# Kernel optimization log

Measured on AMD Instinct MI355X. Metric: run time of the kernel, lower is better.

## Reference

```python
import jax, jax.numpy as jnp
import numpy as np

N_NODES = 40000
N_EDGES = 640000
IN_DIM, H_DIM, OUT_DIM = 128, 128, 64


def setup_inputs() -> dict:
    key = jax.random.key(0)
    ks = jax.random.split(key, 16)
    x = jax.random.normal(ks[0], (N_NODES, IN_DIM), dtype=jnp.float32)
    edge_index = jax.random.randint(ks[1], (2, N_EDGES), 0, N_NODES, dtype=jnp.int64)
    dims = [(IN_DIM, H_DIM), (H_DIM, H_DIM), (H_DIM, OUT_DIM)]
    inp = {"x": x, "edge_index": edge_index}
    for l, (di, do) in enumerate(dims):
        s = 1.0 / np.sqrt(di)
        inp[f"Wr{l}"] = jax.random.uniform(ks[2 + 3 * l], (di, do), jnp.float32, -s, s)  # lin_rel weight
        inp[f"br{l}"] = jax.random.uniform(ks[3 + 3 * l], (do,), jnp.float32, -s, s)     # lin_rel bias
        inp[f"Ws{l}"] = jax.random.uniform(ks[4 + 3 * l], (di, do), jnp.float32, -s, s)  # lin_root weight (no bias)
    return inp


def _graph_conv(x, src, dst, Wr, br, Ws):
    # PyG GraphConv (aggr='add'): out = lin_rel(sum_{j in N(i)} x_j) + lin_root(x_i)
    agg = jax.ops.segment_sum(x[src], dst, num_segments=N_NODES)  # [N, d_in]
    return agg @ Wr + br + x @ Ws


def reference(x, edge_index, Wr0, br0, Ws0, Wr1, br1, Ws1, Wr2, br2, Ws2):
    src, dst = edge_index[0], edge_index[1]
    h = x
    for Wr, br, Ws in ((Wr0, br0, Ws0), (Wr1, br1, Ws1), (Wr2, br2, Ws2)):
        h = _graph_conv(h, src, dst, Wr, br, Ws)
        h = jax.nn.relu(h)
        # dropout p=0 / eval mode -> identity
    return jax.nn.log_softmax(h, axis=1)
```

## Files before the change

### kernel.cpp

```cpp
#include <hip/hip_runtime.h>
#include <hip/hip_bf16.h>


#define N_NODES 40000
#define N_EDGES 640000
#define PAD_NODES 40064
#define DEG_CAP   40960
#define ROW_CAP   64

typedef float v4f __attribute__((ext_vector_type(4)));
typedef float v2f __attribute__((ext_vector_type(2)));
typedef short short8 __attribute__((ext_vector_type(8)));

__device__ inline unsigned short f2b(float f) {
    unsigned u = __float_as_uint(f);
    return (unsigned short)((u + 0x7fffu + ((u >> 16) & 1u)) >> 16);
}

__device__ inline unsigned b2f8(unsigned short us) {
    unsigned s  = ((unsigned)us >> 8) & 0x80u;
    unsigned mag = us & 0x7fffu;
    unsigned e8 = mag >> 7, m7 = mag & 0x7fu;
    unsigned out;
    if (e8 < 121u) out = 0u;
    else if (e8 > 135u) out = 0x7eu;
    else {
        unsigned e4 = e8 - 120u;
        unsigned r  = (m7 + 7u + ((m7 >> 4) & 1u)) >> 4;
        if (r == 8u) { r = 0u; e4++; }
        out = (e4 > 15u || (e4 == 15u && r > 6u)) ? 0x7eu : ((e4 << 3) | r);
    }
    return s | out;
}

#if __has_builtin(__builtin_amdgcn_cvt_f32_fp8)
#define F8TOF(w, sel) __builtin_amdgcn_cvt_f32_fp8((int)(w), (sel))
#else
__device__ inline float f8tof_(unsigned b) {
    unsigned e = (b >> 3) & 15u;
    unsigned bits = ((b & 0x80u) << 24) |
                    (e ? (((e + 120u) << 23) | ((b & 7u) << 20)) : 0u);
    return __uint_as_float(bits);
}
#define F8TOF(w, sel) f8tof_(((unsigned)(w) >> ((sel) * 8)) & 0xffu)
#endif

__global__ __launch_bounds__(256) void prep_kernel(const float* __restrict__ Wr0, const float* __restrict__ Ws0,
                                                   const float* __restrict__ Wr1, const float* __restrict__ Ws1,
                                                   const float* __restrict__ Wr2, const float* __restrict__ Ws2,
                                                   unsigned short* __restrict__ Wt0,
                                                   unsigned short* __restrict__ Wt1,
                                                   unsigned short* __restrict__ Wt2,
                                                   int* __restrict__ deg) {
    int tid = blockIdx.x * 256 + threadIdx.x;
    if (tid < DEG_CAP / 4) {
        ((int4*)deg)[tid] = make_int4(0, 0, 0, 0);
    } else {
        int t = tid - DEG_CAP / 4;
        if (t < 32768) {
            int n = t >> 7, k = t & 127;
            const float* W = (n < 128) ? Wr0 : Ws0;
            Wt0[t] = f2b(W[k * 128 + (n & 127)]);
        } else if (t < 65536) {
            int u = t - 32768;
            int n = u >> 7, k = u & 127;
            const float* W = (n < 128) ? Wr1 : Ws1;
            Wt1[u] = f2b(W[k * 128 + (n & 127)]);
        } else if (t < 81920) {
            int u = t - 65536;
            int n = u >> 7, k = u & 127;
            const float* W = (n < 64) ? Wr2 : Ws2;
            Wt2[u] = f2b(W[k * 64 + (n & 63)]);
        }
    }
}

__global__ __launch_bounds__(256) void place_kernel(const int* __restrict__ src,
                                                    const int* __restrict__ dst,
                                                    int* __restrict__ deg,
                                                    int* __restrict__ esrc) {
    int e = blockIdx.x * 256 + threadIdx.x;
    if (e < N_EDGES) {
        int d = dst[e];
        int r = atomicAdd(&deg[d], 1);
        if (r < ROW_CAP) esrc[(size_t)d * ROW_CAP + r] = src[e];
    }
}

template <int DO, bool F32>
__global__ __launch_bounds__(256, 3) void mm_kernel(const void* __restrict__ Ain,
                                                    const unsigned short* __restrict__ Wt,
                                                    void* __restrict__ Tout,
                                                    unsigned short* __restrict__ S) {
    __shared__ unsigned short Smem[128 * 128];
    unsigned short* As = Smem;
    unsigned short* Bs = Smem + 128 * 64;

    const int tid = threadIdx.x;
    const int m0  = blockIdx.x * 128;
    const int n0  = blockIdx.y * 128;

    const int wave = tid >> 6;
    const int lane = tid & 63;
    const int wr   = (wave >> 1) * 64;
    const int wc   = (wave & 1) * 64;
    const int qm   = lane & 15;
    const int k8   = (lane >> 4) * 8;

    v4f acc[4][4];
#pragma unroll
    for (int i = 0; i < 4; i++)
#pragma unroll
        for (int j = 0; j < 4; j++) acc[i][j] = (v4f)(0.0f);

#pragma unroll
    for (int half = 0; half < 2; half++) {
        if (F32) {
            const float4* Xg = (const float4*)Ain;
#pragma unroll
            for (int i = 0; i < 8; i++) {
                int idx = i * 256 + tid;
                int row = idx >> 4, c4 = idx & 15;
                int gr = m0 + row;
                if (gr > N_NODES - 1) gr = N_NODES - 1;
                float4 v = Xg[(size_t)gr * 32 + half * 16 + c4];
                uint2 p;
                p.x = (unsigned)f2b(v.x) | ((unsigned)f2b(v.y) << 16);
                p.y = (unsigned)f2b(v.z) | ((unsigned)f2b(v.w) << 16);
                ((uint2*)As)[idx] = p;
            }
        } else {
            const unsigned short* Ab = (const unsigned short*)Ain;
#pragma unroll
            for (int i = 0; i < 4; i++) {
                int idx = i * 256 + tid;
                int row = idx >> 3, c8 = idx & 7;
                ((uint4*)As)[idx] =
                    *(const uint4*)(Ab + (size_t)(m0 + row) * 128 + half * 64 + c8 * 8);
            }
        }
        {
#pragma unroll
            for (int i = 0; i < 4; i++) {
                int idx = i * 256 + tid;
                int row = idx >> 3, c8 = idx & 7;
                ((uint4*)Bs)[idx] =
                    *(const uint4*)(Wt + (size_t)(n0 + row) * 128 + half * 64 + c8 * 8);
            }
        }
        __syncthreads();

#pragma unroll
        for (int ks = 0; ks < 2; ks++) {
            short8 af[4], bf[4];
#pragma unroll
            for (int i = 0; i < 4; i++) {
                af[i] = *(const short8*)(const void*)(As + (wr + i * 16 + qm) * 64 + ks * 32 + k8);
                bf[i] = *(const short8*)(const void*)(Bs + (wc + i * 16 + qm) * 64 + ks * 32 + k8);
            }
#pragma unroll
            for (int mi = 0; mi < 4; mi++)
#pragma unroll
                for (int ni = 0; ni < 4; ni++)
                    acc[mi][ni] = __builtin_amdgcn_mfma_f32_16x16x32_bf16(af[mi], bf[ni], acc[mi][ni], 0, 0, 0);
        }
        __syncthreads();
    }

#pragma unroll
    for (int mi = 0; mi < 4; mi++) {
        const int rowBase = wr + mi * 16 + ((lane >> 4) << 2);
#pragma unroll
        for (int r = 0; r < 4; r++) {
            const int row = rowBase + r;
            const int sw  = ((row >> 2) & 3) << 4;
#pragma unroll
            for (int ni = 0; ni < 4; ni++) {
                const int c = wc + ni * 16 + qm;
                Smem[row * 128 + (c ^ sw)] = f2b(acc[mi][ni][r]);
            }
        }
    }
    __syncthreads();

    if (DO == 128 && n0 == 0) {
        unsigned char* T8 = (unsigned char*)Tout;
#pragma unroll
        for (int i = 0; i < 4; i++) {
            const int chunk = i * 256 + tid;
            const int row   = chunk >> 3;
            const int c0    = (chunk & 7) * 16;
            const int sw    = ((row >> 2) & 3) << 4;
            const int node  = m0 + row;
            if (node <= N_NODES) {
                uint4 v = make_uint4(0, 0, 0, 0);
                if (node < N_NODES) {
                    const unsigned short* p = Smem + row * 128 + (c0 ^ sw);
                    unsigned wds[4];
#pragma unroll
                    for (int w4 = 0; w4 < 4; w4++) {
                        wds[w4] =  b2f8(p[w4 * 4 + 0])
                                | (b2f8(p[w4 * 4 + 1]) << 8)
                                | (b2f8(p[w4 * 4 + 2]) << 16)
                                | (b2f8(p[w4 * 4 + 3]) << 24);
                    }
                    v = make_uint4(wds[0], wds[1], wds[2], wds[3]);
                }
                *(uint4*)(T8 + (size_t)node * 128 + c0) = v;
            }
        }
    } else {
        unsigned short* T = (unsigned short*)Tout;
#pragma unroll
        for (int i = 0; i < 8; i++) {
            const int chunk = i * 256 + tid;
            const int row   = chunk >> 4;
            const int c0    = (chunk & 15) * 8;
            const int sw    = ((row >> 2) & 3) << 4;
            const int node  = m0 + row;
            if (node <= N_NODES) {
                uint4 v = make_uint4(0, 0, 0, 0);
                if (node < N_NODES)
                    v = *(const uint4*)(Smem + row * 128 + (c0 ^ sw));
                if (DO == 128) {
                    *(uint4*)(S + (size_t)node * 128 + c0) = v;
                } else {
                    if (c0 < 64) *(uint4*)(T + (size_t)node * 64 + c0) = v;
                    else         *(uint4*)(S + (size_t)node * 64 + (c0 - 64)) = v;
                }
            }
        }
    }
}

__device__ inline void addp(v2f* a, uint4 q) {
    v2f t0 = { __uint_as_float(q.x << 16), __uint_as_float(q.x & 0xffff0000u) };
    v2f t1 = { __uint_as_float(q.y << 16), __uint_as_float(q.y & 0xffff0000u) };
    v2f t2 = { __uint_as_float(q.z << 16), __uint_as_float(q.z & 0xffff0000u) };
    v2f t3 = { __uint_as_float(q.w << 16), __uint_as_float(q.w & 0xffff0000u) };
    a[0] += t0; a[1] += t1; a[2] += t2; a[3] += t3;
}
__device__ inline void addp8(v2f* a, uint2 q) {
    v2f t0 = { F8TOF(q.x, 0), F8TOF(q.x, 1) };
    v2f t1 = { F8TOF(q.x, 2), F8TOF(q.x, 3) };
    v2f t2 = { F8TOF(q.y, 0), F8TOF(q.y, 1) };
    v2f t3 = { F8TOF(q.y, 2), F8TOF(q.y, 3) };
    a[0] += t0; a[1] += t1; a[2] += t2; a[3] += t3;
}

template <int DO, bool LAST, bool FP8T>
__global__ __launch_bounds__(256) void aggregate_kernel(const void* __restrict__ Tin,
                                                        const unsigned short* __restrict__ S,
                                                        const float* __restrict__ br,
                                                        const int* __restrict__ deg,
                                                        const int* __restrict__ esrc,
                                                        unsigned short* __restrict__ Hout,
                                                        float* __restrict__ Fout) {
    constexpr int TPN = DO / 8;
    constexpr int G   = 256 / TPN;
    const int lane = threadIdx.x % TPN;
    const int n    = blockIdx.x * G + threadIdx.x / TPN;

    int cnt = deg[n];
    if (cnt > ROW_CAP) cnt = ROW_CAP;
    const int* erow = esrc + (size_t)n * ROW_CAP;
    const uint4* T4 = (const uint4*)Tin;
    const uint2* T2 = (const uint2*)Tin;

    const uint4  sv = ((const uint4*)S)[(size_t)n * TPN + lane];
    const float4 b0 = ((const float4*)br)[lane * 2];
    const float4 b1 = ((const float4*)br)[lane * 2 + 1];

    v2f acc[4];
    acc[0] = (v2f)(0.0f); acc[1] = (v2f)(0.0f);
    acc[2] = (v2f)(0.0f); acc[3] = (v2f)(0.0f);

    for (int o = 0; o < cnt; o += 8) {
        int4 i0 = *(const int4*)(erow + o);
        int4 i1 = *(const int4*)(erow + o + 4);
        i0.x = (o + 0 < cnt) ? i0.x : N_NODES;
        i0.y = (o + 1 < cnt) ? i0.y : N_NODES;
        i0.z = (o + 2 < cnt) ? i0.z : N_NODES;
        i0.w = (o + 3 < cnt) ? i0.w : N_NODES;
        i1.x = (o + 4 < cnt) ? i1.x : N_NODES;
        i1.y = (o + 5 < cnt) ? i1.y : N_NODES;
        i1.z = (o + 6 < cnt) ? i1.z : N_NODES;
        i1.w = (o + 7 < cnt) ? i1.w : N_NODES;
        if (FP8T) {
            uint2 q0 = T2[(size_t)i0.x * TPN + lane];
            uint2 q1 = T2[(size_t)i0.y * TPN + lane];
            uint2 q2 = T2[(size_t)i0.z * TPN + lane];
            uint2 q3 = T2[(size_t)i0.w * TPN + lane];
            uint2 q4 = T2[(size_t)i1.x * TPN + lane];
            uint2 q5 = T2[(size_t)i1.y * TPN + lane];
            uint2 q6 = T2[(size_t)i1.z * TPN + lane];
            uint2 q7 = T2[(size_t)i1.w * TPN + lane];
            addp8(acc, q0); addp8(acc, q1); addp8(acc, q2); addp8(acc, q3);
            addp8(acc, q4); addp8(acc, q5); addp8(acc, q6); addp8(acc, q7);
        } else {
            uint4 q0 = T4[(size_t)i0.x * TPN + lane];
            uint4 q1 = T4[(size_t)i0.y * TPN + lane];
            uint4 q2 = T4[(size_t)i0.z * TPN + lane];
            uint4 q3 = T4[(size_t)i0.w * TPN + lane];
            uint4 q4 = T4[(size_t)i1.x * TPN + lane];
            uint4 q5 = T4[(size_t)i1.y * TPN + lane];
            uint4 q6 = T4[(size_t)i1.z * TPN + lane];
            uint4 q7 = T4[(size_t)i1.w * TPN + lane];
            addp(acc, q0); addp(acc, q1); addp(acc, q2); addp(acc, q3);
            addp(acc, q4); addp(acc, q5); addp(acc, q6); addp(acc, q7);
        }
    }
    addp(acc, sv);

    float v[8];
    v[0] = fmaxf(acc[0].x + b0.x, 0.f); v[1] = fmaxf(acc[0].y + b0.y, 0.f);
    v[2] = fmaxf(acc[1].x + b0.z, 0.f); v[3] = fmaxf(acc[1].y + b0.w, 0.f);
    v[4] = fmaxf(acc[2].x + b1.x, 0.f); v[5] = fmaxf(acc[2].y + b1.y, 0.f);
    v[6] = fmaxf(acc[3].x + b1.z, 0.f); v[7] = fmaxf(acc[3].y + b1.w, 0.f);

    if (LAST) {
        float m = v[0];
#pragma unroll
        for (int i = 1; i < 8; i++) m = fmaxf(m, v[i]);
#pragma unroll
        for (int off = 4; off; off >>= 1) m = fmaxf(m, __shfl_xor(m, off, 64));
        float es = 0.f;
#pragma unroll
        for (int i = 0; i < 8; i++) es += expf(v[i] - m);
#pragma unroll
        for (int off = 4; off; off >>= 1) es += __shfl_xor(es, off, 64);
        float lse = m + logf(es);
        float4 o0 = make_float4(v[0] - lse, v[1] - lse, v[2] - lse, v[3] - lse);
        float4 o1 = make_float4(v[4] - lse, v[5] - lse, v[6] - lse, v[7] - lse);
        ((float4*)Fout)[(size_t)n * 16 + lane * 2]     = o0;
        ((float4*)Fout)[(size_t)n * 16 + lane * 2 + 1] = o1;
    } else {
        uint4 o;
        o.x = (unsigned)f2b(v[0]) | ((unsigned)f2b(v[1]) << 16);
        o.y = (unsigned)f2b(v[2]) | ((unsigned)f2b(v[3]) << 16);
        o.z = (unsigned)f2b(v[4]) | ((unsigned)f2b(v[5]) << 16);
        o.w = (unsigned)f2b(v[6]) | ((unsigned)f2b(v[7]) << 16);
        ((uint4*)Hout)[(size_t)n * TPN + lane] = o;
    }
}


extern "C" void kernel_launch(void* const* d_in, const int* in_sizes, int n_in,
                              void* d_out, int out_size, void* d_ws, size_t ws_size,
                              hipStream_t stream) {
    const float* x    = (const float*)d_in[0];
    const int*   eidx = (const int*)d_in[1];
    const float* Wr0  = (const float*)d_in[2];
    const float* br0  = (const float*)d_in[3];
    const float* Ws0  = (const float*)d_in[4];
    const float* Wr1  = (const float*)d_in[5];
    const float* br1  = (const float*)d_in[6];
    const float* Ws1  = (const float*)d_in[7];
    const float* Wr2  = (const float*)d_in[8];
    const float* br2  = (const float*)d_in[9];
    const float* Ws2  = (const float*)d_in[10];
    float* out = (float*)d_out;

    const int* src = eidx;
    const int* dst = eidx + N_EDGES;

    auto align = [](size_t v) { return (v + 255) & ~(size_t)255; };
    char* w = (char*)d_ws;
    int* deg  = (int*)w;  w += align(sizeof(int) * DEG_CAP);
    int* esrc = (int*)w;  w += align(sizeof(int) * (size_t)N_NODES * ROW_CAP);
    unsigned short* H1b = (unsigned short*)w;  w += align(2ull * PAD_NODES * 128);
    unsigned short* H2b = (unsigned short*)w;  w += align(2ull * PAD_NODES * 128);
    unsigned short* Wt0 = (unsigned short*)w;  w += align(2ull * 256 * 128);
    unsigned short* Wt1 = (unsigned short*)w;  w += align(2ull * 256 * 128);
    unsigned short* Wt2 = (unsigned short*)w;  w += align(2ull * 128 * 128);
    void*           T   = (void*)w;            w += align(2ull * PAD_NODES * 128);
    unsigned short* Sb  = (unsigned short*)w;  w += align(2ull * PAD_NODES * 128);
    (void)ws_size; (void)n_in; (void)in_sizes; (void)out_size;

    prep_kernel<<<(DEG_CAP / 4 + 81920 + 255) / 256, 256, 0, stream>>>(
        Wr0, Ws0, Wr1, Ws1, Wr2, Ws2, Wt0, Wt1, Wt2, deg);

    place_kernel<<<(N_EDGES + 255) / 256, 256, 0, stream>>>(src, dst, deg, esrc);

    mm_kernel<128, true><<<dim3(PAD_NODES / 128, 2), 256, 0, stream>>>(x, Wt0, T, Sb);
    aggregate_kernel<128, false, true><<<N_NODES / 16, 256, 0, stream>>>(T, Sb, br0, deg, esrc, H1b, nullptr);

    mm_kernel<128, false><<<dim3(PAD_NODES / 128, 2), 256, 0, stream>>>(H1b, Wt1, T, Sb);
    aggregate_kernel<128, false, true><<<N_NODES / 16, 256, 0, stream>>>(T, Sb, br1, deg, esrc, H2b, nullptr);

    mm_kernel<64, false><<<dim3(PAD_NODES / 128, 1), 256, 0, stream>>>(H2b, Wt2, T, Sb);
    aggregate_kernel<64, true, false><<<N_NODES / 32, 256, 0, stream>>>(T, Sb, br2, deg, esrc, nullptr, out);
}
```

Baseline: 212.5 us.

## Pre-convert x to bf16, use hardware fp8 packing, widen aggregate gathers

```diff
diff --git a/kernel.cpp b/kernel.cpp
--- a/kernel.cpp
+++ b/kernel.cpp
@@ -33,6 +33,17 @@
     return s | out;
 }
 
+__device__ inline unsigned pack4_fp8(float f0, float f1, float f2, float f3) {
+#if __has_builtin(__builtin_amdgcn_cvt_pk_fp8_f32)
+    int w = __builtin_amdgcn_cvt_pk_fp8_f32(f0, f1, 0, false);
+    w = __builtin_amdgcn_cvt_pk_fp8_f32(f2, f3, w, true);
+    return (unsigned)w;
+#else
+    return b2f8(f2b(f0)) | (b2f8(f2b(f1)) << 8) |
+           (b2f8(f2b(f2)) << 16) | (b2f8(f2b(f3)) << 24);
+#endif
+}
+
 #if __has_builtin(__builtin_amdgcn_cvt_f32_fp8)
 #define F8TOF(w, sel) __builtin_amdgcn_cvt_f32_fp8((int)(w), (sel))
 #else
@@ -48,29 +59,43 @@
 __global__ __launch_bounds__(256) void prep_kernel(const float* __restrict__ Wr0, const float* __restrict__ Ws0,
                                                    const float* __restrict__ Wr1, const float* __restrict__ Ws1,
                                                    const float* __restrict__ Wr2, const float* __restrict__ Ws2,
+                                                   const float* __restrict__ x,
                                                    unsigned short* __restrict__ Wt0,
                                                    unsigned short* __restrict__ Wt1,
                                                    unsigned short* __restrict__ Wt2,
+                                                   unsigned short* __restrict__ Xb,
                                                    int* __restrict__ deg) {
     int tid = blockIdx.x * 256 + threadIdx.x;
     if (tid < DEG_CAP / 4) {
         ((int4*)deg)[tid] = make_int4(0, 0, 0, 0);
+        return;
+    }
+    int t = tid - DEG_CAP / 4;
+    if (t < 32768) {
+        int n = t >> 7, k = t & 127;
+        const float* W = (n < 128) ? Wr0 : Ws0;
+        Wt0[t] = f2b(W[k * 128 + (n & 127)]);
+    } else if (t < 65536) {
+        int u = t - 32768;
+        int n = u >> 7, k = u & 127;
+        const float* W = (n < 128) ? Wr1 : Ws1;
+        Wt1[u] = f2b(W[k * 128 + (n & 127)]);
+    } else if (t < 81920) {
+        int u = t - 65536;
+        int n = u >> 7, k = u & 127;
+        const float* W = (n < 64) ? Wr2 : Ws2;
+        Wt2[u] = f2b(W[k * 64 + (n & 63)]);
     } else {
-        int t = tid - DEG_CAP / 4;
-        if (t < 32768) {
-            int n = t >> 7, k = t & 127;
-            const float* W = (n < 128) ? Wr0 : Ws0;
-            Wt0[t] = f2b(W[k * 128 + (n & 127)]);
-        } else if (t < 65536) {
-            int u = t - 32768;
-            int n = u >> 7, k = u & 127;
-            const float* W = (n < 128) ? Wr1 : Ws1;
-            Wt1[u] = f2b(W[k * 128 + (n & 127)]);
-        } else if (t < 81920) {
-            int u = t - 65536;
-            int n = u >> 7, k = u & 127;
-            const float* W = (n < 64) ? Wr2 : Ws2;
-            Wt2[u] = f2b(W[k * 64 + (n & 63)]);
+        int u = t - 81920;
+        if (u < (N_NODES * 128) / 8) {
+            float4 a = ((const float4*)x)[u * 2];
+            float4 b = ((const float4*)x)[u * 2 + 1];
+            uint4 o;
+            o.x = (unsigned)f2b(a.x) | ((unsigned)f2b(a.y) << 16);
+            o.y = (unsigned)f2b(a.z) | ((unsigned)f2b(a.w) << 16);
+            o.z = (unsigned)f2b(b.x) | ((unsigned)f2b(b.y) << 16);
+            o.w = (unsigned)f2b(b.z) | ((unsigned)f2b(b.w) << 16);
+            ((uint4*)Xb)[u] = o;
         }
     }
 }
@@ -87,8 +112,8 @@
     }
 }
 
-template <int DO, bool F32>
-__global__ __launch_bounds__(256, 3) void mm_kernel(const void* __restrict__ Ain,
+template <int DO>
+__global__ __launch_bounds__(256, 4) void mm_kernel(const unsigned short* __restrict__ Ab,
                                                     const unsigned short* __restrict__ Wt,
                                                     void* __restrict__ Tout,
                                                     unsigned short* __restrict__ S) {
@@ -115,38 +140,19 @@
 
 #pragma unroll
     for (int half = 0; half < 2; half++) {
-        if (F32) {
-            const float4* Xg = (const float4*)Ain;
-#pragma unroll
-            for (int i = 0; i < 8; i++) {
-                int idx = i * 256 + tid;
-                int row = idx >> 4, c4 = idx & 15;
-                int gr = m0 + row;
-                if (gr > N_NODES - 1) gr = N_NODES - 1;
-                float4 v = Xg[(size_t)gr * 32 + half * 16 + c4];
-                uint2 p;
-                p.x = (unsigned)f2b(v.x) | ((unsigned)f2b(v.y) << 16);
-                p.y = (unsigned)f2b(v.z) | ((unsigned)f2b(v.w) << 16);
-                ((uint2*)As)[idx] = p;
-            }
-        } else {
-            const unsigned short* Ab = (const unsigned short*)Ain;
-#pragma unroll
-            for (int i = 0; i < 4; i++) {
-                int idx = i * 256 + tid;
-                int row = idx >> 3, c8 = idx & 7;
-                ((uint4*)As)[idx] =
-                    *(const uint4*)(Ab + (size_t)(m0 + row) * 128 + half * 64 + c8 * 8);
-            }
-        }
-        {
-#pragma unroll
-            for (int i = 0; i < 4; i++) {
-                int idx = i * 256 + tid;
-                int row = idx >> 3, c8 = idx & 7;
-                ((uint4*)Bs)[idx] =
-                    *(const uint4*)(Wt + (size_t)(n0 + row) * 128 + half * 64 + c8 * 8);
-            }
+#pragma unroll
+        for (int i = 0; i < 4; i++) {
+            int idx = i * 256 + tid;
+            int row = idx >> 3, c8 = idx & 7;
+            ((uint4*)As)[idx] =
+                *(const uint4*)(Ab + (size_t)(m0 + row) * 128 + half * 64 + c8 * 8);
+        }
+#pragma unroll
+        for (int i = 0; i < 4; i++) {
+            int idx = i * 256 + tid;
+            int row = idx >> 3, c8 = idx & 7;
+            ((uint4*)Bs)[idx] =
+                *(const uint4*)(Wt + (size_t)(n0 + row) * 128 + half * 64 + c8 * 8);
         }
         __syncthreads();
 
@@ -196,15 +202,16 @@
                 uint4 v = make_uint4(0, 0, 0, 0);
                 if (node < N_NODES) {
                     const unsigned short* p = Smem + row * 128 + (c0 ^ sw);
-                    unsigned wds[4];
-#pragma unroll
-                    for (int w4 = 0; w4 < 4; w4++) {
-                        wds[w4] =  b2f8(p[w4 * 4 + 0])
-                                | (b2f8(p[w4 * 4 + 1]) << 8)
-                                | (b2f8(p[w4 * 4 + 2]) << 16)
-                                | (b2f8(p[w4 * 4 + 3]) << 24);
-                    }
-                    v = make_uint4(wds[0], wds[1], wds[2], wds[3]);
+                    uint4 ha = *(const uint4*)p;
+                    uint4 hb = *(const uint4*)(p + 8);
+#define LOF(d) __uint_as_float((d) << 16)
+#define HIF(d) __uint_as_float((d) & 0xffff0000u)
+                    v.x = pack4_fp8(LOF(ha.x), HIF(ha.x), LOF(ha.y), HIF(ha.y));
+                    v.y = pack4_fp8(LOF(ha.z), HIF(ha.z), LOF(ha.w), HIF(ha.w));
+                    v.z = pack4_fp8(LOF(hb.x), HIF(hb.x), LOF(hb.y), HIF(hb.y));
+                    v.w = pack4_fp8(LOF(hb.z), HIF(hb.z), LOF(hb.w), HIF(hb.w));
+#undef LOF
+#undef HIF
                 }
                 *(uint4*)(T8 + (size_t)node * 128 + c0) = v;
             }
@@ -240,12 +247,14 @@
     v2f t3 = { __uint_as_float(q.w << 16), __uint_as_float(q.w & 0xffff0000u) };
     a[0] += t0; a[1] += t1; a[2] += t2; a[3] += t3;
 }
-__device__ inline void addp8(v2f* a, uint2 q) {
-    v2f t0 = { F8TOF(q.x, 0), F8TOF(q.x, 1) };
-    v2f t1 = { F8TOF(q.x, 2), F8TOF(q.x, 3) };
-    v2f t2 = { F8TOF(q.y, 0), F8TOF(q.y, 1) };
-    v2f t3 = { F8TOF(q.y, 2), F8TOF(q.y, 3) };
-    a[0] += t0; a[1] += t1; a[2] += t2; a[3] += t3;
+__device__ inline void addp8w(v2f* a, unsigned w) {
+    v2f t0 = { F8TOF(w, 0), F8TOF(w, 1) };
+    v2f t1 = { F8TOF(w, 2), F8TOF(w, 3) };
+    a[0] += t0; a[1] += t1;
+}
+__device__ inline void addp16(v2f* a, uint4 q) {
+    addp8w(a + 0, q.x); addp8w(a + 2, q.y);
+    addp8w(a + 4, q.z); addp8w(a + 6, q.w);
 }
 
 template <int DO, bool LAST, bool FP8T>
@@ -256,7 +265,8 @@
                                                         const int* __restrict__ esrc,
                                                         unsigned short* __restrict__ Hout,
                                                         float* __restrict__ Fout) {
-    constexpr int TPN = DO / 8;
+    constexpr int TPN = 8;
+    constexpr int DPL = DO / TPN;
     constexpr int G   = 256 / TPN;
     const int lane = threadIdx.x % TPN;
     const int n    = blockIdx.x * G + threadIdx.x / TPN;
@@ -265,15 +275,10 @@
     if (cnt > ROW_CAP) cnt = ROW_CAP;
     const int* erow = esrc + (size_t)n * ROW_CAP;
     const uint4* T4 = (const uint4*)Tin;
-    const uint2* T2 = (const uint2*)Tin;
-
-    const uint4  sv = ((const uint4*)S)[(size_t)n * TPN + lane];
-    const float4 b0 = ((const float4*)br)[lane * 2];
-    const float4 b1 = ((const float4*)br)[lane * 2 + 1];
-
-    v2f acc[4];
-    acc[0] = (v2f)(0.0f); acc[1] = (v2f)(0.0f);
-    acc[2] = (v2f)(0.0f); acc[3] = (v2f)(0.0f);
+
+    v2f acc[DPL / 2];
+#pragma unroll
+    for (int i = 0; i < DPL / 2; i++) acc[i] = (v2f)(0.0f);
 
     for (int o = 0; o < cnt; o += 8) {
         int4 i0 = *(const int4*)(erow + o);
@@ -286,37 +291,34 @@
         i1.y = (o + 5 < cnt) ? i1.y : N_NODES;
         i1.z = (o + 6 < cnt) ? i1.z : N_NODES;
         i1.w = (o + 7 < cnt) ? i1.w : N_NODES;
+        uint4 q0 = T4[(size_t)i0.x * TPN + lane];
+        uint4 q1 = T4[(size_t)i0.y * TPN + lane];
+        uint4 q2 = T4[(size_t)i0.z * TPN + lane];
+        uint4 q3 = T4[(size_t)i0.w * TPN + lane];
+        uint4 q4 = T4[(size_t)i1.x * TPN + lane];
+        uint4 q5 = T4[(size_t)i1.y * TPN + lane];
+        uint4 q6 = T4[(size_t)i1.z * TPN + lane];
+        uint4 q7 = T4[(size_t)i1.w * TPN + lane];
         if (FP8T) {
-            uint2 q0 = T2[(size_t)i0.x * TPN + lane];
-            uint2 q1 = T2[(size_t)i0.y * TPN + lane];
-            uint2 q2 = T2[(size_t)i0.z * TPN + lane];
-            uint2 q3 = T2[(size_t)i0.w * TPN + lane];
-            uint2 q4 = T2[(size_t)i1.x * TPN + lane];
-            uint2 q5 = T2[(size_t)i1.y * TPN + lane];
-            uint2 q6 = T2[(size_t)i1.z * TPN + lane];
-            uint2 q7 = T2[(size_t)i1.w * TPN + lane];
-            addp8(acc, q0); addp8(acc, q1); addp8(acc, q2); addp8(acc, q3);
-            addp8(acc, q4); addp8(acc, q5); addp8(acc, q6); addp8(acc, q7);
+            addp16(acc, q0); addp16(acc, q1); addp16(acc, q2); addp16(acc, q3);
+            addp16(acc, q4); addp16(acc, q5); addp16(acc, q6); addp16(acc, q7);
         } else {
-            uint4 q0 = T4[(size_t)i0.x * TPN + lane];
-            uint4 q1 = T4[(size_t)i0.y * TPN + lane];
-            uint4 q2 = T4[(size_t)i0.z * TPN + lane];
-            uint4 q3 = T4[(size_t)i0.w * TPN + lane];
-            uint4 q4 = T4[(size_t)i1.x * TPN + lane];
-            uint4 q5 = T4[(size_t)i1.y * TPN + lane];
-            uint4 q6 = T4[(size_t)i1.z * TPN + lane];
-            uint4 q7 = T4[(size_t)i1.w * TPN + lane];
             addp(acc, q0); addp(acc, q1); addp(acc, q2); addp(acc, q3);
             addp(acc, q4); addp(acc, q5); addp(acc, q6); addp(acc, q7);
         }
     }
-    addp(acc, sv);
-
-    float v[8];
-    v[0] = fmaxf(acc[0].x + b0.x, 0.f); v[1] = fmaxf(acc[0].y + b0.y, 0.f);
-    v[2] = fmaxf(acc[1].x + b0.z, 0.f); v[3] = fmaxf(acc[1].y + b0.w, 0.f);
-    v[4] = fmaxf(acc[2].x + b1.x, 0.f); v[5] = fmaxf(acc[2].y + b1.y, 0.f);
-    v[6] = fmaxf(acc[3].x + b1.z, 0.f); v[7] = fmaxf(acc[3].y + b1.w, 0.f);
+
+    float v[DPL];
+#pragma unroll
+    for (int h = 0; h < DPL / 8; h++) {
+        uint4 sv = ((const uint4*)S)[(size_t)n * (DO / 8) + lane * (DPL / 8) + h];
+        addp(acc + h * 4, sv);
+    }
+#pragma unroll
+    for (int j = 0; j < DPL; j++) {
+        float bj = br[lane * DPL + j];
+        v[j] = fmaxf(((j & 1) ? acc[j >> 1].y : acc[j >> 1].x) + bj, 0.f);
+    }
 
     if (LAST) {
         float m = v[0];
@@ -335,12 +337,15 @@
         ((float4*)Fout)[(size_t)n * 16 + lane * 2]     = o0;
         ((float4*)Fout)[(size_t)n * 16 + lane * 2 + 1] = o1;
     } else {
-        uint4 o;
-        o.x = (unsigned)f2b(v[0]) | ((unsigned)f2b(v[1]) << 16);
-        o.y = (unsigned)f2b(v[2]) | ((unsigned)f2b(v[3]) << 16);
-        o.z = (unsigned)f2b(v[4]) | ((unsigned)f2b(v[5]) << 16);
-        o.w = (unsigned)f2b(v[6]) | ((unsigned)f2b(v[7]) << 16);
-        ((uint4*)Hout)[(size_t)n * TPN + lane] = o;
+#pragma unroll
+        for (int h = 0; h < DPL / 8; h++) {
+            uint4 o;
+            o.x = (unsigned)f2b(v[h * 8 + 0]) | ((unsigned)f2b(v[h * 8 + 1]) << 16);
+            o.y = (unsigned)f2b(v[h * 8 + 2]) | ((unsigned)f2b(v[h * 8 + 3]) << 16);
+            o.z = (unsigned)f2b(v[h * 8 + 4]) | ((unsigned)f2b(v[h * 8 + 5]) << 16);
+            o.w = (unsigned)f2b(v[h * 8 + 6]) | ((unsigned)f2b(v[h * 8 + 7]) << 16);
+            ((uint4*)Hout)[(size_t)n * (DO / 8) + lane * (DPL / 8) + h] = o;
+        }
     }
 }
 
@@ -368,6 +373,7 @@
     char* w = (char*)d_ws;
     int* deg  = (int*)w;  w += align(sizeof(int) * DEG_CAP);
     int* esrc = (int*)w;  w += align(sizeof(int) * (size_t)N_NODES * ROW_CAP);
+    unsigned short* Xb  = (unsigned short*)w;  w += align(2ull * PAD_NODES * 128);
     unsigned short* H1b = (unsigned short*)w;  w += align(2ull * PAD_NODES * 128);
     unsigned short* H2b = (unsigned short*)w;  w += align(2ull * PAD_NODES * 128);
     unsigned short* Wt0 = (unsigned short*)w;  w += align(2ull * 256 * 128);
@@ -377,17 +383,17 @@
     unsigned short* Sb  = (unsigned short*)w;  w += align(2ull * PAD_NODES * 128);
     (void)ws_size; (void)n_in; (void)in_sizes; (void)out_size;
 
-    prep_kernel<<<(DEG_CAP / 4 + 81920 + 255) / 256, 256, 0, stream>>>(
-        Wr0, Ws0, Wr1, Ws1, Wr2, Ws2, Wt0, Wt1, Wt2, deg);
+    prep_kernel<<<(DEG_CAP / 4 + 81920 + (N_NODES * 128) / 8 + 255) / 256, 256, 0, stream>>>(
+        Wr0, Ws0, Wr1, Ws1, Wr2, Ws2, x, Wt0, Wt1, Wt2, Xb, deg);
 
     place_kernel<<<(N_EDGES + 255) / 256, 256, 0, stream>>>(src, dst, deg, esrc);
 
-    mm_kernel<128, true><<<dim3(PAD_NODES / 128, 2), 256, 0, stream>>>(x, Wt0, T, Sb);
-    aggregate_kernel<128, false, true><<<N_NODES / 16, 256, 0, stream>>>(T, Sb, br0, deg, esrc, H1b, nullptr);
-
-    mm_kernel<128, false><<<dim3(PAD_NODES / 128, 2), 256, 0, stream>>>(H1b, Wt1, T, Sb);
-    aggregate_kernel<128, false, true><<<N_NODES / 16, 256, 0, stream>>>(T, Sb, br1, deg, esrc, H2b, nullptr);
-
-    mm_kernel<64, false><<<dim3(PAD_NODES / 128, 1), 256, 0, stream>>>(H2b, Wt2, T, Sb);
+    mm_kernel<128><<<dim3(PAD_NODES / 128, 2), 256, 0, stream>>>(Xb, Wt0, T, Sb);
+    aggregate_kernel<128, false, true><<<N_NODES / 32, 256, 0, stream>>>(T, Sb, br0, deg, esrc, H1b, nullptr);
+
+    mm_kernel<128><<<dim3(PAD_NODES / 128, 2), 256, 0, stream>>>(H1b, Wt1, T, Sb);
+    aggregate_kernel<128, false, true><<<N_NODES / 32, 256, 0, stream>>>(T, Sb, br1, deg, esrc, H2b, nullptr);
+
+    mm_kernel<64><<<dim3(PAD_NODES / 128, 1), 256, 0, stream>>>(H2b, Wt2, T, Sb);
     aggregate_kernel<64, true, false><<<N_NODES / 32, 256, 0, stream>>>(T, Sb, br2, deg, esrc, nullptr, out);
 }
```

New measurement: 203.3 us. 4.4% less time.
